# Kernel tuning notes

Measured on AMD Instinct MI355X. Metric: run time of the kernel, lower is better.

## Reference

```python
import jax, jax.numpy as jnp
import numpy as np

NUM_HEADS = 4

def setup_inputs() -> dict:
    key = jax.random.key(0)
    ks = jax.random.split(key, 7)
    B, Lq, Lk, E, D, LAT = 16, 256, 4096, 64, 32, 32
    query = jax.random.normal(ks[0], (B, Lq, E), dtype=jnp.float32)
    key_in = jax.random.normal(ks[1], (B, Lk, E), dtype=jnp.float32)
    value = jax.random.normal(ks[2], (B, Lk, D), dtype=jnp.float32)
    mask = jax.random.randint(ks[3], (B, Lk, D), 0, 2, dtype=jnp.int32)
    Wq = jax.random.normal(ks[4], (E, E), dtype=jnp.float32) / np.sqrt(E).astype(np.float32)
    bq = jnp.zeros((E,), dtype=jnp.float32)
    Wk = jax.random.normal(ks[5], (E, E), dtype=jnp.float32) / np.sqrt(E).astype(np.float32)
    bk = jnp.zeros((E,), dtype=jnp.float32)
    Wo = jax.random.normal(ks[6], (NUM_HEADS * D, LAT), dtype=jnp.float32) / np.sqrt(NUM_HEADS * D).astype(np.float32)
    bo = jnp.zeros((LAT,), dtype=jnp.float32)
    return {"query": query, "key": key_in, "value": value, "mask": mask,
            "Wq": Wq, "bq": bq, "Wk": Wk, "bk": bk, "Wo": Wo, "bo": bo}

def reference(query, key, value, mask, Wq, bq, Wk, bk, Wo, bo):
    B, Lk, D = value.shape
    Lq = query.shape[1]
    h = NUM_HEADS
    ek = query.shape[-1] // h  # embed_time_k
    # linear maps (torch Linear: y = x @ W; here W stored as (in, out))
    q = (query @ Wq + bq).reshape(B, Lq, h, ek).transpose(0, 2, 1, 3)  # (B,h,Lq,ek)
    k = (key @ Wk + bk).reshape(B, Lk, h, ek).transpose(0, 2, 1, 3)    # (B,h,Lk,ek)
    scores = jnp.einsum('bhqe,bhke->bhqk', q, k) / jnp.sqrt(jnp.asarray(ek, q.dtype))
    # Original repeats scores over D, masks per-feature with -inf, softmaxes over Lk,
    # then does a weighted sum. Equivalent fused form (never builds (B,h,Lq,Lk,D)):
    e = jnp.exp(scores - jnp.max(scores, axis=-1, keepdims=True))  # (B,h,Lq,Lk)
    m = mask.astype(value.dtype)                                   # (B,Lk,D) 0/1
    num = jnp.einsum('bhqk,bkd->bhqd', e, m * value)
    den = jnp.einsum('bhqk,bkd->bhqd', e, m)
    x = num / den                                                  # (B,h,Lq,D)
    x = x.transpose(0, 2, 1, 3).reshape(B, Lq, h * D)
    return x @ Wo + bo  # (B, Lq, latent_dim)
```

## Files before the change

### kernel.cpp

```cpp
#include <hip/hip_runtime.h>
#include <hip/hip_bf16.h>
#include <math.h>

typedef __bf16 bf16;
typedef bf16 bf16x4 __attribute__((ext_vector_type(4)));
typedef bf16 bf16x8 __attribute__((ext_vector_type(8)));
typedef float f32x4 __attribute__((ext_vector_type(4)));

#define B_   16
#define LQ_  256
#define LK_  4096
#define E_   64
#define H_   4
#define EK_  16
#define D_   32
#define LAT_ 32

#define OFF_QP    0u
#define OFF_KP    524288u
#define OFF_MVFB  8912896u
#define OFF_WOT   17301504u
#define OFF_ND    17309696u
#define WS_NEED   21504000u

#define LOG2E 1.44269504f

__device__ inline f32x4 mfma_bf16(bf16x8 a, bf16x8 b, f32x4 c) {
  return __builtin_amdgcn_mfma_f32_16x16x32_bf16(a, b, c, 0, 0, 0);
}
__device__ inline bf16x8 zero8() {
  bf16x8 z;
#pragma unroll
  for (int i = 0; i < 8; ++i) z[i] = (bf16)0.0f;
  return z;
}

__global__ __launch_bounds__(256) void prep_kernel(
    const float* __restrict__ query, const float* __restrict__ key,
    const float* __restrict__ value, const int* __restrict__ mask,
    const float* __restrict__ Wq, const float* __restrict__ bq,
    const float* __restrict__ Wk, const float* __restrict__ bk,
    const float* __restrict__ Wo,
    bf16* __restrict__ qp, bf16* __restrict__ kp,
    bf16* __restrict__ mvfB, bf16* __restrict__ WoT)
{
  __shared__ __align__(16) bf16 s_b[16896];
  const int bid = blockIdx.x;
  const int tid = threadIdx.x;

  if (bid < 544) {
    const bool isQ = bid < 32;
    const int row0 = isQ ? bid * 128 : (bid - 32) * 128;
    const float* in   = isQ ? query : key;
    const float* W    = isQ ? Wq : Wk;
    const float* bias = isQ ? bq : bk;
    bf16* outp        = isQ ? qp : kp;
    const float scal  = isQ ? (0.25f * LOG2E) : 1.0f;

    bf16* sIn = s_b;
    bf16* sWT = s_b + 9216;

#pragma unroll
    for (int p = 0; p < 8; ++p) {
      int f4 = tid + p * 256;
      int row = f4 >> 4, e4 = (f4 & 15) * 4;
      float4 v = *(const float4*)(in + (size_t)(row0 + row) * 64 + e4);
      bf16x4 b4;
      b4[0] = (bf16)v.x; b4[1] = (bf16)v.y; b4[2] = (bf16)v.z; b4[3] = (bf16)v.w;
      *(bf16x4*)(sIn + row * 72 + e4) = b4;
    }
#pragma unroll
    for (int p = 0; p < 4; ++p) {
      int f4 = tid + p * 256;
      int k = f4 >> 4, c4 = (f4 & 15) * 4;
      float4 v = *(const float4*)(W + k * 64 + c4);
      sWT[(c4 + 0) * 72 + k] = (bf16)v.x;
      sWT[(c4 + 1) * 72 + k] = (bf16)v.y;
      sWT[(c4 + 2) * 72 + k] = (bf16)v.z;
      sWT[(c4 + 3) * 72 + k] = (bf16)v.w;
    }
    __syncthreads();

    const int w = tid >> 6, l = tid & 63, l15 = l & 15, g = l >> 4;
    f32x4 acc[2][4];
#pragma unroll
    for (int mt = 0; mt < 2; ++mt)
#pragma unroll
      for (int nt = 0; nt < 4; ++nt) acc[mt][nt] = f32x4{0.f, 0.f, 0.f, 0.f};

#pragma unroll
    for (int ks = 0; ks < 2; ++ks) {
      bf16x8 A0 = *(bf16x8*)(sIn + (32 * w + l15) * 72 + 32 * ks + 8 * g);
      bf16x8 A1 = *(bf16x8*)(sIn + (32 * w + 16 + l15) * 72 + 32 * ks + 8 * g);
#pragma unroll
      for (int nt = 0; nt < 4; ++nt) {
        bf16x8 Bf = *(bf16x8*)(sWT + (16 * nt + l15) * 72 + 32 * ks + 8 * g);
        acc[0][nt] = mfma_bf16(A0, Bf, acc[0][nt]);
        acc[1][nt] = mfma_bf16(A1, Bf, acc[1][nt]);
      }
    }
#pragma unroll
    for (int mt = 0; mt < 2; ++mt)
#pragma unroll
      for (int nt = 0; nt < 4; ++nt) {
        int col = 16 * nt + l15;
        float bv = bias[col];
#pragma unroll
        for (int r = 0; r < 4; ++r) {
          int row = row0 + 32 * w + 16 * mt + 4 * g + r;
          outp[(size_t)row * 64 + col] = (bf16)((acc[mt][nt][r] + bv) * scal);
        }
      }
  } else if (bid < 800) {
    const int rb = bid - 544;
    const int b = rb >> 4, kk0 = (rb & 15) * 256;
#pragma unroll
    for (int p = 0; p < 8; ++p) {
      int f4 = tid + p * 256;
      int kk = f4 >> 3, d4 = (f4 & 7) * 4;
      size_t gi = ((size_t)(b * LK_ + kk0 + kk)) * 32 + d4;
      float4 v = *(const float4*)(value + gi);
      int4   m = *(const int4*)(mask + gi);
      s_b[(d4 + 0) * 264 + kk] = (bf16)(m.x ? v.x : 0.0f);
      s_b[(d4 + 1) * 264 + kk] = (bf16)(m.y ? v.y : 0.0f);
      s_b[(d4 + 2) * 264 + kk] = (bf16)(m.z ? v.z : 0.0f);
      s_b[(d4 + 3) * 264 + kk] = (bf16)(m.w ? v.w : 0.0f);
      s_b[(32 + d4 + 0) * 264 + kk] = (bf16)(float)m.x;
      s_b[(32 + d4 + 1) * 264 + kk] = (bf16)(float)m.y;
      s_b[(32 + d4 + 2) * 264 + kk] = (bf16)(float)m.z;
      s_b[(32 + d4 + 3) * 264 + kk] = (bf16)(float)m.w;
    }
    __syncthreads();
    const int col = tid >> 2, seg = tid & 3;
    const int nt = col >> 4, l15c = col & 15;
#pragma unroll
    for (int w2 = 0; w2 < 8; ++w2) {
      int kkg = seg * 64 + w2 * 8;
      int tile = (kk0 + kkg) >> 5;
      int gq = (kkg >> 3) & 3;
      int lane = 16 * gq + l15c;
      uint4 d = *(uint4*)(s_b + col * 264 + kkg);
      *(uint4*)(mvfB + (size_t)((((b * 128 + tile) * 4 + nt) * 64 + lane)) * 8) = d;
    }
  } else {
#pragma unroll
    for (int p = 0; p < 16; ++p) {
      int f = tid + p * 256;
      int k = f >> 5, n = f & 31;
      WoT[n * 128 + k] = (bf16)Wo[f];
    }
  }
}

__global__ __launch_bounds__(256, 4) void attn_kernel(
    const bf16* __restrict__ qp, const bf16* __restrict__ kp,
    const bf16* __restrict__ mvfB, float* __restrict__ nd)
{
  __shared__ __align__(16) bf16 s_se[5120];

  const int bid = blockIdx.x;
  const int kc = bid & 7, qt = (bid >> 3) & 7, b = bid >> 6;
  const int tid = threadIdx.x;
  const int w = tid >> 6, l = tid & 63, l15 = l & 15, g = l >> 4;
  const int q0 = qt * 32;
  const int tile0 = kc * 16;

  bf16x8 qB[2];
  if (l < 32) {
#pragma unroll
    for (int nt = 0; nt < 2; ++nt) {
      int q = q0 + 16 * nt + l15;
      qB[nt] = *(const bf16x8*)(qp + (size_t)((b * LQ_ + q) * 64 + w * EK_ + g * 8));
    }
  } else { qB[0] = zero8(); qB[1] = zero8(); }

  f32x4 acc[2][4];
#pragma unroll
  for (int mt = 0; mt < 2; ++mt)
#pragma unroll
    for (int nt = 0; nt < 4; ++nt) acc[mt][nt] = f32x4{0.f, 0.f, 0.f, 0.f};

  bf16* se_w = s_se + w * 1280;
  const bf16* mvt0 = mvfB + (size_t)(b * 128 + tile0) * 2048;

#pragma unroll 2
  for (int t = 0; t < 16; ++t) {
    const int kk0 = (tile0 + t) * 32;
    const bf16* mvt = mvt0 + (size_t)t * 2048;

    bf16x8 mvB[4];
#pragma unroll
    for (int nt = 0; nt < 4; ++nt)
      mvB[nt] = *(const bf16x8*)(mvt + (nt * 64 + l) * 8);

    bf16x8 kA0, kA1;
    if (l < 32) {
      kA0 = *(const bf16x8*)(kp + (size_t)((b * LK_ + kk0 + l15) * 64 + w * EK_ + g * 8));
      kA1 = *(const bf16x8*)(kp + (size_t)((b * LK_ + kk0 + 16 + l15) * 64 + w * EK_ + g * 8));
    } else { kA0 = zero8(); kA1 = zero8(); }

    f32x4 S[2][2];
    S[0][0] = mfma_bf16(kA0, qB[0], f32x4{0.f, 0.f, 0.f, 0.f});
    S[0][1] = mfma_bf16(kA0, qB[1], f32x4{0.f, 0.f, 0.f, 0.f});
    S[1][0] = mfma_bf16(kA1, qB[0], f32x4{0.f, 0.f, 0.f, 0.f});
    S[1][1] = mfma_bf16(kA1, qB[1], f32x4{0.f, 0.f, 0.f, 0.f});

#pragma unroll
    for (int mt = 0; mt < 2; ++mt)
#pragma unroll
      for (int nt = 0; nt < 2; ++nt) {
        f32x4 s = S[mt][nt];
        bf16x4 e4;
#pragma unroll
        for (int r = 0; r < 4; ++r) e4[r] = (bf16)exp2f(s[r]);
        *(bf16x4*)(se_w + (16 * nt + l15) * 40 + 16 * mt + 4 * g) = e4;
      }

    asm volatile("" ::: "memory");

    bf16x8 eA0 = *(bf16x8*)(se_w + l15 * 40 + 8 * g);
    bf16x8 eA1 = *(bf16x8*)(se_w + (16 + l15) * 40 + 8 * g);

#pragma unroll
    for (int nt = 0; nt < 4; ++nt) {
      acc[0][nt] = mfma_bf16(eA0, mvB[nt], acc[0][nt]);
      acc[1][nt] = mfma_bf16(eA1, mvB[nt], acc[1][nt]);
    }
  }

#pragma unroll
  for (int mt = 0; mt < 2; ++mt)
#pragma unroll
    for (int nt = 0; nt < 4; ++nt)
#pragma unroll
      for (int r = 0; r < 4; ++r) {
        int q = q0 + 16 * mt + 4 * g + r;
        int col = 16 * nt + l15;
        atomicAdd(&nd[(size_t)((b * 4 + w) * LQ_ + q) * 64 + col], acc[mt][nt][r]);
      }
}

__global__ __launch_bounds__(256) void out_kernel(
    const float* __restrict__ nd, const bf16* __restrict__ WoT,
    const float* __restrict__ bo, float* __restrict__ out)
{
  __shared__ __align__(16) bf16 s_x[16 * 136];
  const int bid = blockIdx.x;
  const int b = bid >> 4, q0 = (bid & 15) * 16;
  const int tid = threadIdx.x;
  const int q = tid >> 4, jg = tid & 15;
#pragma unroll
  for (int jj = 0; jj < 8; ++jj) {
    int j = jg * 8 + jj;
    int h = j >> 5, d = j & 31;
    size_t base = (size_t)((b * 4 + h) * LQ_ + q0 + q) * 64;
    float num = nd[base + d], den = nd[base + 32 + d];
    s_x[q * 136 + j] = (bf16)(num / den);
  }
  __syncthreads();
  const int w = tid >> 6, l = tid & 63, l15 = l & 15, g = l >> 4;
  if (w < 2) {
    const int nt = w;
    f32x4 acc = f32x4{0.f, 0.f, 0.f, 0.f};
#pragma unroll
    for (int ks = 0; ks < 4; ++ks) {
      bf16x8 A  = *(bf16x8*)(s_x + l15 * 136 + 32 * ks + 8 * g);
      bf16x8 Bf = *(const bf16x8*)(WoT + (l15 + 16 * nt) * 128 + 32 * ks + 8 * g);
      acc = mfma_bf16(A, Bf, acc);
    }
    float bv = bo[l15 + 16 * nt];
#pragma unroll
    for (int r = 0; r < 4; ++r) {
      int row = q0 + 4 * g + r;
      out[(size_t)(b * LQ_ + row) * LAT_ + l15 + 16 * nt] = acc[r] + bv;
    }
  }
}

extern "C" void kernel_launch(void* const* d_in, const int* in_sizes, int n_in,
                              void* d_out, int out_size, void* d_ws, size_t ws_size,
                              hipStream_t stream) {
  const float* query = (const float*)d_in[0];
  const float* key   = (const float*)d_in[1];
  const float* value = (const float*)d_in[2];
  const int*   mask  = (const int*)d_in[3];
  const float* Wq    = (const float*)d_in[4];
  const float* bq    = (const float*)d_in[5];
  const float* Wk    = (const float*)d_in[6];
  const float* bk    = (const float*)d_in[7];
  const float* Wo    = (const float*)d_in[8];
  const float* bo    = (const float*)d_in[9];
  float* out = (float*)d_out;
  char* ws = (char*)d_ws;

  if (ws_size < (size_t)WS_NEED) return;

  bf16* qp   = (bf16*)(ws + OFF_QP);
  bf16* kp   = (bf16*)(ws + OFF_KP);
  bf16* mvfB = (bf16*)(ws + OFF_MVFB);
  bf16* WoT  = (bf16*)(ws + OFF_WOT);
  float* nd  = (float*)(ws + OFF_ND);

  hipMemsetAsync(nd, 0, 4194304u, stream);
  prep_kernel<<<801, 256, 0, stream>>>(query, key, value, mask, Wq, bq, Wk, bk,
                                       Wo, qp, kp, mvfB, WoT);
  attn_kernel<<<1024, 256, 0, stream>>>(qp, kp, mvfB, nd);
  out_kernel<<<256, 256, 0, stream>>>(nd, WoT, bo, out);
}
```

Before: 139.7 us.

## Fuse attention and output projection into one kernel, dropping atomics and memset

Replaces the split-K attention kernel (1024 blocks, atomicAdd into a global num/den buffer) and the separate output kernel with a single kernel of 256 blocks of 512 threads. Each block handles 16 queries with all 4 heads and two key halves, reduces the halves through shared memory, and then applies the Wo projection in place. This removes the memset, the global atomics and one launch. The cost is far fewer blocks (256 across the GPU) with each wave looping over 64 tiles serially, which lowers parallelism and latency hiding. Each mvfB tile is also now read once per 16 queries instead of once per 32.

```diff
diff --git a/kernel.cpp b/kernel.cpp
--- a/kernel.cpp
+++ b/kernel.cpp
@@ -20,8 +20,7 @@
 #define OFF_KP    524288u
 #define OFF_MVFB  8912896u
 #define OFF_WOT   17301504u
-#define OFF_ND    17309696u
-#define WS_NEED   21504000u
+#define WS_NEED   17309696u
 
 #define LOG2E 1.44269504f
 
@@ -152,40 +151,38 @@
   }
 }
 
-__global__ __launch_bounds__(256, 4) void attn_kernel(
+__global__ __launch_bounds__(512, 2) void fused_attn(
     const bf16* __restrict__ qp, const bf16* __restrict__ kp,
-    const bf16* __restrict__ mvfB, float* __restrict__ nd)
+    const bf16* __restrict__ mvfB, const bf16* __restrict__ WoT,
+    const float* __restrict__ bo, float* __restrict__ out)
 {
-  __shared__ __align__(16) bf16 s_se[5120];
+  __shared__ __align__(16) bf16  s_se[8 * 640];
+  __shared__ __align__(16) float s_acc[4 * 16 * 65];
+  __shared__ __align__(16) bf16  s_x[16 * 136];
 
   const int bid = blockIdx.x;
-  const int kc = bid & 7, qt = (bid >> 3) & 7, b = bid >> 6;
+  const int b = bid >> 4, qt = bid & 15;
+  const int q0 = qt * 16;
   const int tid = threadIdx.x;
   const int w = tid >> 6, l = tid & 63, l15 = l & 15, g = l >> 4;
-  const int q0 = qt * 32;
-  const int tile0 = kc * 16;
-
-  bf16x8 qB[2];
+  const int h = w & 3, s = w >> 2;
+  const int tile0 = s * 64;
+
+  bf16x8 qB;
   if (l < 32) {
-#pragma unroll
-    for (int nt = 0; nt < 2; ++nt) {
-      int q = q0 + 16 * nt + l15;
-      qB[nt] = *(const bf16x8*)(qp + (size_t)((b * LQ_ + q) * 64 + w * EK_ + g * 8));
-    }
-  } else { qB[0] = zero8(); qB[1] = zero8(); }
-
-  f32x4 acc[2][4];
-#pragma unroll
-  for (int mt = 0; mt < 2; ++mt)
-#pragma unroll
-    for (int nt = 0; nt < 4; ++nt) acc[mt][nt] = f32x4{0.f, 0.f, 0.f, 0.f};
-
-  bf16* se_w = s_se + w * 1280;
+    qB = *(const bf16x8*)(qp + (size_t)((b * LQ_ + q0 + l15) * 64 + h * EK_ + g * 8));
+  } else { qB = zero8(); }
+
+  f32x4 acc[4];
+#pragma unroll
+  for (int nt = 0; nt < 4; ++nt) acc[nt] = f32x4{0.f, 0.f, 0.f, 0.f};
+
+  bf16* se_w = s_se + w * 640;
   const bf16* mvt0 = mvfB + (size_t)(b * 128 + tile0) * 2048;
+  const bf16* kp_b = kp + (size_t)(b * LK_ + tile0 * 32) * 64 + h * EK_ + g * 8;
 
 #pragma unroll 2
-  for (int t = 0; t < 16; ++t) {
-    const int kk0 = (tile0 + t) * 32;
+  for (int t = 0; t < 64; ++t) {
     const bf16* mvt = mvt0 + (size_t)t * 2048;
 
     bf16x8 mvB[4];
@@ -195,84 +192,64 @@
 
     bf16x8 kA0, kA1;
     if (l < 32) {
-      kA0 = *(const bf16x8*)(kp + (size_t)((b * LK_ + kk0 + l15) * 64 + w * EK_ + g * 8));
-      kA1 = *(const bf16x8*)(kp + (size_t)((b * LK_ + kk0 + 16 + l15) * 64 + w * EK_ + g * 8));
+      kA0 = *(const bf16x8*)(kp_b + (size_t)(t * 32 + l15) * 64);
+      kA1 = *(const bf16x8*)(kp_b + (size_t)(t * 32 + 16 + l15) * 64);
     } else { kA0 = zero8(); kA1 = zero8(); }
 
-    f32x4 S[2][2];
-    S[0][0] = mfma_bf16(kA0, qB[0], f32x4{0.f, 0.f, 0.f, 0.f});
-    S[0][1] = mfma_bf16(kA0, qB[1], f32x4{0.f, 0.f, 0.f, 0.f});
-    S[1][0] = mfma_bf16(kA1, qB[0], f32x4{0.f, 0.f, 0.f, 0.f});
-    S[1][1] = mfma_bf16(kA1, qB[1], f32x4{0.f, 0.f, 0.f, 0.f});
-
-#pragma unroll
-    for (int mt = 0; mt < 2; ++mt)
-#pragma unroll
-      for (int nt = 0; nt < 2; ++nt) {
-        f32x4 s = S[mt][nt];
-        bf16x4 e4;
-#pragma unroll
-        for (int r = 0; r < 4; ++r) e4[r] = (bf16)exp2f(s[r]);
-        *(bf16x4*)(se_w + (16 * nt + l15) * 40 + 16 * mt + 4 * g) = e4;
+    f32x4 S0 = mfma_bf16(kA0, qB, f32x4{0.f, 0.f, 0.f, 0.f});
+    f32x4 S1 = mfma_bf16(kA1, qB, f32x4{0.f, 0.f, 0.f, 0.f});
+
+    bf16x4 e0, e1;
+#pragma unroll
+    for (int r = 0; r < 4; ++r) { e0[r] = (bf16)exp2f(S0[r]); e1[r] = (bf16)exp2f(S1[r]); }
+    *(bf16x4*)(se_w + l15 * 40 + 4 * g)      = e0;
+    *(bf16x4*)(se_w + l15 * 40 + 16 + 4 * g) = e1;
+
+    asm volatile("" ::: "memory");
+
+    bf16x8 eA = *(bf16x8*)(se_w + l15 * 40 + 8 * g);
+
+#pragma unroll
+    for (int nt = 0; nt < 4; ++nt)
+      acc[nt] = mfma_bf16(eA, mvB[nt], acc[nt]);
+  }
+
+  if (s == 1) {
+    float* pa = s_acc + h * 1040;
+#pragma unroll
+    for (int nt = 0; nt < 4; ++nt)
+#pragma unroll
+      for (int r = 0; r < 4; ++r)
+        pa[(4 * g + r) * 65 + 16 * nt + l15] = acc[nt][r];
+  }
+  __syncthreads();
+  if (s == 0) {
+    const float* pa = s_acc + h * 1040;
+#pragma unroll
+    for (int nt = 0; nt < 2; ++nt)
+#pragma unroll
+      for (int r = 0; r < 4; ++r) {
+        int q = 4 * g + r, dcol = 16 * nt + l15;
+        float num = acc[nt][r]     + pa[q * 65 + dcol];
+        float den = acc[nt + 2][r] + pa[q * 65 + dcol + 32];
+        s_x[q * 136 + h * 32 + dcol] = (bf16)(num / den);
       }
-
-    asm volatile("" ::: "memory");
-
-    bf16x8 eA0 = *(bf16x8*)(se_w + l15 * 40 + 8 * g);
-    bf16x8 eA1 = *(bf16x8*)(se_w + (16 + l15) * 40 + 8 * g);
-
-#pragma unroll
-    for (int nt = 0; nt < 4; ++nt) {
-      acc[0][nt] = mfma_bf16(eA0, mvB[nt], acc[0][nt]);
-      acc[1][nt] = mfma_bf16(eA1, mvB[nt], acc[1][nt]);
-    }
-  }
-
-#pragma unroll
-  for (int mt = 0; mt < 2; ++mt)
-#pragma unroll
-    for (int nt = 0; nt < 4; ++nt)
-#pragma unroll
-      for (int r = 0; r < 4; ++r) {
-        int q = q0 + 16 * mt + 4 * g + r;
-        int col = 16 * nt + l15;
-        atomicAdd(&nd[(size_t)((b * 4 + w) * LQ_ + q) * 64 + col], acc[mt][nt][r]);
-      }
-}
-
-__global__ __launch_bounds__(256) void out_kernel(
-    const float* __restrict__ nd, const bf16* __restrict__ WoT,
-    const float* __restrict__ bo, float* __restrict__ out)
-{
-  __shared__ __align__(16) bf16 s_x[16 * 136];
-  const int bid = blockIdx.x;
-  const int b = bid >> 4, q0 = (bid & 15) * 16;
-  const int tid = threadIdx.x;
-  const int q = tid >> 4, jg = tid & 15;
-#pragma unroll
-  for (int jj = 0; jj < 8; ++jj) {
-    int j = jg * 8 + jj;
-    int h = j >> 5, d = j & 31;
-    size_t base = (size_t)((b * 4 + h) * LQ_ + q0 + q) * 64;
-    float num = nd[base + d], den = nd[base + 32 + d];
-    s_x[q * 136 + j] = (bf16)(num / den);
   }
   __syncthreads();
-  const int w = tid >> 6, l = tid & 63, l15 = l & 15, g = l >> 4;
   if (w < 2) {
     const int nt = w;
-    f32x4 acc = f32x4{0.f, 0.f, 0.f, 0.f};
+    f32x4 oacc = f32x4{0.f, 0.f, 0.f, 0.f};
 #pragma unroll
     for (int ks = 0; ks < 4; ++ks) {
       bf16x8 A  = *(bf16x8*)(s_x + l15 * 136 + 32 * ks + 8 * g);
       bf16x8 Bf = *(const bf16x8*)(WoT + (l15 + 16 * nt) * 128 + 32 * ks + 8 * g);
-      acc = mfma_bf16(A, Bf, acc);
+      oacc = mfma_bf16(A, Bf, oacc);
     }
     float bv = bo[l15 + 16 * nt];
 #pragma unroll
     for (int r = 0; r < 4; ++r) {
       int row = q0 + 4 * g + r;
-      out[(size_t)(b * LQ_ + row) * LAT_ + l15 + 16 * nt] = acc[r] + bv;
+      out[(size_t)(b * LQ_ + row) * LAT_ + l15 + 16 * nt] = oacc[r] + bv;
     }
   }
 }
@@ -299,11 +276,8 @@
   bf16* kp   = (bf16*)(ws + OFF_KP);
   bf16* mvfB = (bf16*)(ws + OFF_MVFB);
   bf16* WoT  = (bf16*)(ws + OFF_WOT);
-  float* nd  = (float*)(ws + OFF_ND);
-
-  hipMemsetAsync(nd, 0, 4194304u, stream);
+
   prep_kernel<<<801, 256, 0, stream>>>(query, key, value, mask, Wq, bq, Wk, bk,
                                        Wo, qp, kp, mvfB, WoT);
-  attn_kernel<<<1024, 256, 0, stream>>>(qp, kp, mvfB, nd);
-  out_kernel<<<256, 256, 0, stream>>>(nd, WoT, bo, out);
-}
+  fused_attn<<<256, 512, 0, stream>>>(qp, kp, mvfB, WoT, bo, out);
+}
```

Result: faster. 131.5 us (-5.9%).
